# Optimization experiments

Measured on AMD Instinct MI355X. Metric: run time of the kernel, lower is better.

## Reference

```python
import jax, jax.numpy as jnp
import numpy as np

EPS = 1e-5
EMBED_DIM = 1024
CTX_DIM = 768
NUM_HEADS = 16
DH = EMBED_DIM // NUM_HEADS
# Faithful to torch source: embed_dim // num_heads ** 0.5 parses as embed_dim // (num_heads**0.5)
SCALE = EMBED_DIM // (NUM_HEADS ** 0.5)  # = 256.0


def ws_conv1x1(x, w, b, mask):
    # weight-standardized 1x1 conv1d: w [O, I, 1], x [B, I, T]
    w2 = w[..., 0]
    mu = jnp.mean(w2, axis=1, keepdims=True)
    var = jnp.var(w2, axis=1, keepdims=True)
    wn = (w2 - mu) * jax.lax.rsqrt(var + EPS)
    y = jnp.einsum('oi,bit->bot', wn, x) + b[None, :, None]
    if mask is not None:
        y = jnp.where(mask, y, 0.0)  # mask [B,1,T] bool
    return y


def layernorm(x, g, b):
    # normalize over last axis
    mu = jnp.mean(x, axis=-1, keepdims=True)
    var = jnp.var(x, axis=-1, keepdims=True)
    return (x - mu) * jax.lax.rsqrt(var + EPS) * g + b


def setup_inputs() -> dict:
    key = jax.random.key(0)
    ks = jax.random.split(key, 16)
    B, T, S = 4, 1024, 1024
    inp = {
        'x': jax.random.normal(ks[0], (B, EMBED_DIM, T), dtype=jnp.float32),
        'context': jax.random.normal(ks[1], (B, CTX_DIM, S), dtype=jnp.float32),
        'mask': jax.random.randint(ks[2], (B, 1, T), 0, 2).astype(bool),
        'mask_ctx': jax.random.randint(ks[3], (B, 1, S), 0, 2).astype(bool),
        'qw': jax.random.normal(ks[4], (EMBED_DIM, EMBED_DIM, 1), dtype=jnp.float32) * 0.02,
        'qb': jnp.zeros((EMBED_DIM,), jnp.float32),
        'kw': jax.random.normal(ks[5], (EMBED_DIM, CTX_DIM, 1), dtype=jnp.float32) * 0.02,
        'kb': jnp.zeros((EMBED_DIM,), jnp.float32),
        'vw': jax.random.normal(ks[6], (EMBED_DIM, CTX_DIM, 1), dtype=jnp.float32) * 0.02,
        'vb': jnp.zeros((EMBED_DIM,), jnp.float32),
        'ow': jax.random.normal(ks[7], (EMBED_DIM, EMBED_DIM, 1), dtype=jnp.float32) * 0.02,
        'ob': jnp.zeros((EMBED_DIM,), jnp.float32),
        'gq': jnp.ones((DH,), jnp.float32), 'bq': jnp.zeros((DH,), jnp.float32),
        'gk': jnp.ones((DH,), jnp.float32), 'bk': jnp.zeros((DH,), jnp.float32),
        'gv': jnp.ones((DH,), jnp.float32), 'bv': jnp.zeros((DH,), jnp.float32),
    }
    return inp


def reference(x, context, mask, mask_ctx, qw, qb, kw, kb, vw, vb, ow, ob, gq, bq, gk, bk, gv, bv):
    B, E, T = x.shape
    S = context.shape[-1]
    q = ws_conv1x1(x, qw, qb, mask)            # [B,E,T]
    k = ws_conv1x1(context, kw, kb, mask_ctx)  # [B,E,S]
    v = ws_conv1x1(context, vw, vb, mask_ctx)  # [B,E,S]
    # split heads -> [B,H,dh,L]
    q = q.reshape(B, NUM_HEADS, DH, T)
    k = k.reshape(B, NUM_HEADS, DH, S)
    v = v.reshape(B, NUM_HEADS, DH, S)
    # middle_norm: LayerNorm over dh (applied on transposed layout)
    q = jnp.swapaxes(layernorm(jnp.swapaxes(q, -1, -2), gq, bq), -1, -2)
    k = jnp.swapaxes(layernorm(jnp.swapaxes(k, -1, -2), gk, bk), -1, -2)
    v = jnp.swapaxes(layernorm(jnp.swapaxes(v, -1, -2), gv, bv), -1, -2)
    # scores: k^T @ q -> [B,H,S,T]
    scores = jnp.einsum('bhds,bhdt->bhst', k, q) / SCALE
    scores = jnp.where(mask[:, :, None, :], scores, -1e9)  # mask over query dim T
    scores = jax.nn.softmax(scores, axis=-1)               # softmax over T (as in source)
    scores = jnp.where(mask_ctx[:, :, :, None], scores, 0.0)
    out = jnp.einsum('bhds,bhst->bhdt', v, scores)          # v @ scores -> [B,H,dh,T]
    out = out.reshape(B, E, T)
    out = ws_conv1x1(out, ow, ob, mask) + x
    return out
```

## Files before the change

### kernel.cpp

```cpp
#include <hip/hip_runtime.h>

#define NB 4
#define TT 1024
#define SS 1024
#define EE 1024
#define CCH 768
#define NH 16
#define DHH 64
#define EPSF 1e-5f
#define QSCALE (1.4426950408889634f / 256.0f)

typedef unsigned short u16;
typedef __attribute__((ext_vector_type(8))) short short8;
typedef __attribute__((ext_vector_type(8))) unsigned short u16x8;
typedef __attribute__((ext_vector_type(4))) unsigned short u16x4;
typedef __attribute__((ext_vector_type(4))) float f32x4;

__device__ __forceinline__ u16 f2bu(float f) {
    union { float f; unsigned u; } x; x.f = f;
    unsigned r = x.u + 0x7fffu + ((x.u >> 16) & 1u);
    return (u16)(r >> 16);
}
__device__ __forceinline__ float bu2f(u16 u) {
    union { unsigned u; float f; } x; x.u = ((unsigned)u) << 16; return x.f;
}

#if __has_builtin(__builtin_amdgcn_exp2f)
#define EXP2(x) __builtin_amdgcn_exp2f(x)
#else
#define EXP2(x) exp2f(x)
#endif

#define MFMA16(a, b, c) __builtin_amdgcn_mfma_f32_16x16x32_bf16((a), (b), (c), 0, 0, 0)

__global__ __launch_bounds__(256) void ws_norm_scan(
    const float* __restrict__ qw, const float* __restrict__ kw,
    const float* __restrict__ vw, const float* __restrict__ ow,
    u16* __restrict__ wqn, u16* __restrict__ wkn,
    u16* __restrict__ wvn, u16* __restrict__ won,
    const int* __restrict__ mask, const int* __restrict__ mask_ctx,
    int* __restrict__ tIdx, int* __restrict__ sIdx,
    int* __restrict__ cntQ, int* __restrict__ cntK) {
    int tid = threadIdx.x;
    if (blockIdx.y == 4) {
        if (blockIdx.x >= 8) return;
        int which = blockIdx.x & 1, b = blockIdx.x >> 1;
        const int* m = (which ? mask_ctx : mask) + b * 1024;
        int* idx = (which ? sIdx : tIdx) + b * 1024;
        int* cnt = (which ? cntK : cntQ) + b;
        int base = tid * 4;
        int v[4]; int s = 0;
#pragma unroll
        for (int i = 0; i < 4; i++) { v[i] = m[base + i] ? 1 : 0; s += v[i]; }
        int lane = tid & 63, wid = tid >> 6;
        int inc = s;
#pragma unroll
        for (int off = 1; off < 64; off <<= 1) {
            int o = __shfl_up(inc, off);
            if (lane >= off) inc += o;
        }
        __shared__ int wtot[4];
        if (lane == 63) wtot[wid] = inc;
        __syncthreads();
        int woff = 0;
        for (int i = 0; i < wid; i++) woff += wtot[i];
        int p = woff + inc - s;
#pragma unroll
        for (int i = 0; i < 4; i++) {
            if (v[i]) idx[p] = base + i;
            p += v[i];
        }
        if (tid == 255) *cnt = p;
        return;
    }
    int mat = blockIdx.y;
    const float* w = mat == 0 ? qw : (mat == 1 ? kw : (mat == 2 ? vw : ow));
    u16* wn = mat == 0 ? wqn : (mat == 1 ? wkn : (mat == 2 ? wvn : won));
    int I = (mat == 1 || mat == 2) ? CCH : EE;
    int row = blockIdx.x;
    const float* wr = w + (size_t)row * I;
    float s = 0.f, s2 = 0.f;
    for (int i = tid; i < I; i += 256) { float v = wr[i]; s += v; s2 += v * v; }
#pragma unroll
    for (int off = 32; off > 0; off >>= 1) { s += __shfl_down(s, off); s2 += __shfl_down(s2, off); }
    __shared__ float sa[4], sb[4], smean, srstd;
    int wid = tid >> 6;
    if ((tid & 63) == 0) { sa[wid] = s; sb[wid] = s2; }
    __syncthreads();
    if (tid == 0) {
        float ts = sa[0] + sa[1] + sa[2] + sa[3];
        float ts2 = sb[0] + sb[1] + sb[2] + sb[3];
        float mean = ts / (float)I;
        float var = ts2 / (float)I - mean * mean;
        smean = mean; srstd = rsqrtf(var + EPSF);
    }
    __syncthreads();
    float mean = smean, r = srstd;
    u16* wo = wn + (size_t)row * I;
    for (int i = tid; i < I; i += 256) wo[i] = f2bu((wr[i] - mean) * r);
}

__global__ __launch_bounds__(256) void transpose2_compact(
    const float* __restrict__ x, const float* __restrict__ ctx,
    const int* __restrict__ mask, const int* __restrict__ mask_ctx,
    u16* __restrict__ xc, u16* __restrict__ cc) {
    __shared__ float tile[64][65];
    __shared__ int spos[64], smask[64], wtot[4];
    int yy = blockIdx.y;
    int mat = yy < 16 ? 0 : 1;
    int r0 = (mat == 0 ? yy : yy - 16) * 64;
    int R = mat == 0 ? EE : CCH;
    const float* in = mat == 0 ? x : ctx;
    const int* m = (mat == 0 ? mask : mask_ctx) + (size_t)blockIdx.z * 1024;
    u16* out = mat == 0 ? xc : cc;
    int c0 = blockIdx.x * 64, b = blockIdx.z;
    const float* ip = in + (size_t)b * R * 1024;
    u16* op = out + (size_t)b * R * 1024;
    int tid = threadIdx.x;
#pragma unroll
    for (int mm = 0; mm < 16; mm++) {
        int id = tid + 256 * mm; int r = id >> 6, c = id & 63;
        tile[r][c] = ip[(size_t)(r0 + r) * 1024 + c0 + c];
    }
    int base = tid * 4;
    int v[4]; int s = 0;
#pragma unroll
    for (int i = 0; i < 4; i++) { v[i] = m[base + i] ? 1 : 0; s += v[i]; }
    int lane = tid & 63, wid = tid >> 6;
    int inc = s;
#pragma unroll
    for (int off = 1; off < 64; off <<= 1) {
        int o = __shfl_up(inc, off);
        if (lane >= off) inc += o;
    }
    if (lane == 63) wtot[wid] = inc;
    __syncthreads();
    int woff = 0;
    for (int i = 0; i < wid; i++) woff += wtot[i];
    int p = woff + inc - s;
#pragma unroll
    for (int i = 0; i < 4; i++) {
        int g = base + i;
        if (g >= c0 && g < c0 + 64) { spos[g - c0] = p; smask[g - c0] = v[i]; }
        p += v[i];
    }
    __syncthreads();
#pragma unroll
    for (int mm = 0; mm < 16; mm++) {
        int id = tid + 256 * mm; int rr = id >> 6, cc2 = id & 63;
        if (smask[rr])
            op[(size_t)spos[rr] * R + r0 + cc2] = f2bu(tile[cc2][rr]);
    }
}

__device__ __forceinline__ void gemm_core(
    const u16* __restrict__ A, const u16* __restrict__ Bp, int I,
    int o0, int l0, u16 (*at)[72], u16 (*bt)[72], f32x4 (&acc)[4][2]) {
    int tid = threadIdx.x;
    int w = tid >> 6, lane = tid & 63, quad = lane >> 4, l16 = lane & 15;
    int wm = w & 1, wn = w >> 1;
    int rA = tid >> 3, cA = (tid & 7) * 8;
    u16x8 ra[2][4], rb[2][2];
#pragma unroll
    for (int p = 0; p < 2; p++) {
        int kb = p * 64;
#pragma unroll
        for (int m = 0; m < 4; m++)
            ra[p][m] = *(const u16x8*)&A[(size_t)(o0 + rA + 32 * m) * I + kb + cA];
#pragma unroll
        for (int m = 0; m < 2; m++)
            rb[p][m] = *(const u16x8*)&Bp[(size_t)(l0 + rA + 32 * m) * I + kb + cA];
    }
    for (int k0 = 0; k0 < I; k0 += 128) {
#pragma unroll
        for (int half = 0; half < 2; half++) {
            __syncthreads();
#pragma unroll
            for (int m = 0; m < 4; m++) *(u16x8*)&at[rA + 32 * m][cA] = ra[half][m];
#pragma unroll
            for (int m = 0; m < 2; m++) *(u16x8*)&bt[rA + 32 * m][cA] = rb[half][m];
            __syncthreads();
            int kpre = k0 + half * 64 + 128;
            if (kpre < I) {
#pragma unroll
                for (int m = 0; m < 4; m++)
                    ra[half][m] = *(const u16x8*)&A[(size_t)(o0 + rA + 32 * m) * I + kpre + cA];
#pragma unroll
                for (int m = 0; m < 2; m++)
                    rb[half][m] = *(const u16x8*)&Bp[(size_t)(l0 + rA + 32 * m) * I + kpre + cA];
            }
#pragma unroll
            for (int ks = 0; ks < 64; ks += 32) {
                short8 af[4], bf[2];
#pragma unroll
                for (int i = 0; i < 4; i++)
                    af[i] = *(const short8*)&at[wm * 64 + i * 16 + l16][ks + quad * 8];
#pragma unroll
                for (int j = 0; j < 2; j++)
                    bf[j] = *(const short8*)&bt[wn * 32 + j * 16 + l16][ks + quad * 8];
#pragma unroll
                for (int mt = 0; mt < 4; mt++)
#pragma unroll
                    for (int nt = 0; nt < 2; nt++)
                        acc[mt][nt] = MFMA16(af[mt], bf[nt], acc[mt][nt]);
            }
        }
    }
}

__global__ __launch_bounds__(256) void proj_qkv(
    const u16* __restrict__ wq, const u16* __restrict__ wk, const u16* __restrict__ wv,
    const u16* __restrict__ xc, const u16* __restrict__ cc,
    const float* __restrict__ qb, const float* __restrict__ kb, const float* __restrict__ vbi,
    const int* __restrict__ cntQ, const int* __restrict__ cntK,
    const float* __restrict__ gq, const float* __restrict__ bq,
    const float* __restrict__ gk, const float* __restrict__ bk,
    u16* __restrict__ qc, u16* __restrict__ kc, u16* __restrict__ yv) {
    int mat = blockIdx.y >> 3;
    int l0 = blockIdx.x * 64;
    int b = blockIdx.z;
    int limit = (mat == 0) ? cntQ[b] : cntK[b];
    if (l0 >= limit) return;
    __shared__ u16 at[128][72];
    __shared__ u16 bt[64][72];
    __shared__ float sg[64], sbe[64], sbias[128];
    int tid = threadIdx.x;
    int w = tid >> 6, lane = tid & 63, quad = lane >> 4, l16 = lane & 15;
    int wm = w & 1, wn = w >> 1;
    int o0 = (blockIdx.y & 7) * 128;
    const u16* A = mat == 0 ? wq : (mat == 1 ? wk : wv);
    const u16* BT = mat == 0 ? xc : cc;
    const float* bias = mat == 0 ? qb : (mat == 1 ? kb : vbi);
    int I = mat == 0 ? EE : CCH;
    if (mat < 2 && tid < 64) {
        sg[tid] = (mat == 0 ? gq : gk)[tid];
        sbe[tid] = (mat == 0 ? bq : bk)[tid];
    }
    if (tid < 128) sbias[tid] = bias[o0 + tid];

    f32x4 acc[4][2] = {};
    gemm_core(A, BT + (size_t)b * 1024 * I, I, o0, l0, at, bt, acc);

    if (mat < 2) {
        u16* outT = mat == 0 ? qc : kc;
        float scale = mat == 0 ? QSCALE : 1.0f;
        int h = (o0 >> 6) + wm;
        int bh = b * NH + h;
#pragma unroll
        for (int nt = 0; nt < 2; nt++) {
            int l = l0 + wn * 32 + nt * 16 + l16;
            float vbuf[16];
            float s = 0.f;
#pragma unroll
            for (int mt = 0; mt < 4; mt++)
#pragma unroll
                for (int reg = 0; reg < 4; reg++) {
                    float v = acc[mt][nt][reg] + sbias[wm * 64 + mt * 16 + quad * 4 + reg];
                    vbuf[mt * 4 + reg] = v; s += v;
                }
            s += __shfl_xor(s, 16); s += __shfl_xor(s, 32);
            float mean = s * (1.f / 64);
            float s2 = 0.f;
#pragma unroll
            for (int i = 0; i < 16; i++) { float dv = vbuf[i] - mean; s2 += dv * dv; }
            s2 += __shfl_xor(s2, 16); s2 += __shfl_xor(s2, 32);
            float r = rsqrtf(s2 * (1.f / 64) + EPSF);
            if (l < limit) {
                u16* op = outT + ((size_t)bh * 1024 + l) * 64;
#pragma unroll
                for (int mt = 0; mt < 4; mt++) {
                    u16x4 pk;
#pragma unroll
                    for (int reg = 0; reg < 4; reg++) {
                        int d = mt * 16 + quad * 4 + reg;
                        pk[reg] = f2bu(((vbuf[mt * 4 + reg] - mean) * r * sg[d] + sbe[d]) * scale);
                    }
                    *(u16x4*)&op[mt * 16 + quad * 4] = pk;
                }
            }
        }
    } else {
#pragma unroll
        for (int nt = 0; nt < 2; nt++) {
            int l = l0 + wn * 32 + nt * 16 + l16;
            if (l < limit) {
#pragma unroll
                for (int mt = 0; mt < 4; mt++)
#pragma unroll
                    for (int reg = 0; reg < 4; reg++) {
                        int o = o0 + wm * 64 + mt * 16 + quad * 4 + reg;
                        float v = acc[mt][nt][reg] + sbias[wm * 64 + mt * 16 + quad * 4 + reg];
                        yv[((size_t)b * EE + o) * 1024 + l] = f2bu(v);
                    }
            }
        }
    }
}

__global__ __launch_bounds__(256) void proj_o(
    const u16* __restrict__ won, const u16* __restrict__ aT,
    const float* __restrict__ obi, const int* __restrict__ mask,
    const float* __restrict__ x, float* __restrict__ out) {
    __shared__ u16 at[128][72];
    __shared__ u16 bt[64][72];
    __shared__ float sbias[128];
    int tid = threadIdx.x;
    int w = tid >> 6, lane = tid & 63, quad = lane >> 4, l16 = lane & 15;
    int wm = w & 1, wn = w >> 1;
    int o0 = blockIdx.y * 128, l0 = blockIdx.x * 64, b = blockIdx.z;
    if (tid < 128) sbias[tid] = obi[o0 + tid];
    f32x4 acc[4][2] = {};
    gemm_core(won, aT + (size_t)b * TT * EE, EE, o0, l0, at, bt, acc);
    const int* mrow = mask + (size_t)b * TT;
#pragma unroll
    for (int nt = 0; nt < 2; nt++) {
        int l = l0 + wn * 32 + nt * 16 + l16;
        int mval = mrow[l];
#pragma unroll
        for (int mt = 0; mt < 4; mt++)
#pragma unroll
            for (int reg = 0; reg < 4; reg++) {
                int o = o0 + wm * 64 + mt * 16 + quad * 4 + reg;
                float v = mval ? (acc[mt][nt][reg] + sbias[wm * 64 + mt * 16 + quad * 4 + reg]) : 0.f;
                size_t off = ((size_t)b * EE + o) * TT + l;
                out[off] = v + x[off];
            }
    }
}

__global__ __launch_bounds__(256) void attn_stats_mfma(
    const u16* __restrict__ qc, const u16* __restrict__ kc,
    const int* __restrict__ cntQ, const int* __restrict__ cntK,
    const float* __restrict__ gv, const float* __restrict__ bv,
    const u16* __restrict__ yv, u16* __restrict__ vc) {
    int s0 = blockIdx.x * 64, h = blockIdx.y, b = blockIdx.z;
    int Sc = cntK[b], Tc = cntQ[b];
    if (s0 >= Sc) return;
    __shared__ u16 kt[64][72];
    __shared__ u16 qt[64][72];
    __shared__ float lp[4][64];
    int tid = threadIdx.x;
    int w = tid >> 6, lane = tid & 63, quad = lane >> 4, l16 = lane & 15;
    int head = b * NH + h;
    const u16* kp = kc + (size_t)head * SS * DHH;
    const u16* qp = qc + (size_t)head * TT * DHH;
    int rA = tid >> 3, cA = (tid & 7) * 8;
#pragma unroll
    for (int m = 0; m < 2; m++)
        *(u16x8*)&kt[rA + 32 * m][cA] = *(const u16x8*)&kp[(size_t)(s0 + rA + 32 * m) * DHH + cA];
    u16x8 rq[2][2];
#pragma unroll
    for (int p = 0; p < 2; p++)
#pragma unroll
        for (int m = 0; m < 2; m++)
            rq[p][m] = *(const u16x8*)&qp[(size_t)(p * 64 + rA + 32 * m) * DHH + cA];
    float rl[4][4] = {};
    for (int t0 = 0; t0 < Tc; t0 += 128) {
#pragma unroll
        for (int half = 0; half < 2; half++) {
            int tb = t0 + half * 64;
            __syncthreads();
#pragma unroll
            for (int m = 0; m < 2; m++) *(u16x8*)&qt[rA + 32 * m][cA] = rq[half][m];
            __syncthreads();
            int tpre = tb + 128;
            if (tpre < TT) {
#pragma unroll
                for (int m = 0; m < 2; m++)
                    rq[half][m] = *(const u16x8*)&qp[(size_t)(tpre + rA + 32 * m) * DHH + cA];
            }
            int tcol = tb + w * 16 + l16;
            f32x4 acc[4] = {};
#pragma unroll
            for (int ks = 0; ks < 64; ks += 32) {
                short8 bf = *(const short8*)&qt[w * 16 + l16][ks + quad * 8];
#pragma unroll
                for (int mt = 0; mt < 4; mt++) {
                    short8 af = *(const short8*)&kt[mt * 16 + l16][ks + quad * 8];
                    acc[mt] = MFMA16(af, bf, acc[mt]);
                }
            }
            if (tcol < Tc) {
#pragma unroll
                for (int mt = 0; mt < 4; mt++)
#pragma unroll
                    for (int reg = 0; reg < 4; reg++)
                        rl[mt][reg] += EXP2(acc[mt][reg]);
            }
        }
    }
#pragma unroll
    for (int mt = 0; mt < 4; mt++) {
#pragma unroll
        for (int reg = 0; reg < 4; reg++) {
            float v = rl[mt][reg];
            v += __shfl_xor(v, 1); v += __shfl_xor(v, 2);
            v += __shfl_xor(v, 4); v += __shfl_xor(v, 8);
            if (l16 == 0) lp[w][mt * 16 + quad * 4 + reg] = v;
        }
    }
    __syncthreads();
    if (tid < 64 && s0 + tid < Sc) {
        int spos = s0 + tid;
        float lv = lp[0][tid] + lp[1][tid] + lp[2][tid] + lp[3][tid];
        float wsc = lv > 0.f ? (1.f / lv) : 0.f;
        const u16* vin = yv + ((size_t)b * EE + h * 64) * SS + spos;
        u16* vout = vc + ((size_t)b * EE + h * 64) * SS + spos;
        float sm = 0.f, s2 = 0.f;
        float vals[DHH];
#pragma unroll
        for (int d = 0; d < DHH; d++) {
            float v = bu2f(vin[(size_t)d * SS]);
            vals[d] = v; sm += v; s2 += v * v;
        }
        float mean = sm * (1.f / DHH);
        float var = s2 * (1.f / DHH) - mean * mean;
        float r = rsqrtf(var + EPSF);
#pragma unroll
        for (int d = 0; d < DHH; d++)
            vout[(size_t)d * SS] = f2bu(((vals[d] - mean) * r * gv[d] + bv[d]) * wsc);
    }
}

__global__ __launch_bounds__(256) void attn_pv_mfma(
    const u16* __restrict__ qc, const u16* __restrict__ kc, const u16* __restrict__ vc,
    const int* __restrict__ tIdx, const int* __restrict__ cntQ, const int* __restrict__ cntK,
    u16* __restrict__ aT) {
    int t0 = blockIdx.x * 64, h = blockIdx.y, b = blockIdx.z;
    int Tc = cntQ[b], Sc = cntK[b];
    if (t0 >= Tc) return;
    __shared__ u16 qt[64][72];
    __shared__ u16 kt[64][72];
    __shared__ u16 vt[64][72];
    __shared__ u16 pt[64][72];
    int tid = threadIdx.x;
    int w = tid >> 6, lane = tid & 63, quad = lane >> 4, l16 = lane & 15;
    int head = b * NH + h;
    const u16* qp = qc + (size_t)head * TT * DHH;
    const u16* kp = kc + (size_t)head * SS * DHH;
    const u16* vp = vc + ((size_t)head * DHH) * SS;
    int rA = tid >> 3, cA = (tid & 7) * 8;
#pragma unroll
    for (int m = 0; m < 2; m++)
        *(u16x8*)&qt[rA + 32 * m][cA] = *(const u16x8*)&qp[(size_t)(t0 + rA + 32 * m) * DHH + cA];
    u16x8 rk[2][2], rv[2][2];
#pragma unroll
    for (int p = 0; p < 2; p++)
#pragma unroll
        for (int m = 0; m < 2; m++) {
            rk[p][m] = *(const u16x8*)&kp[(size_t)(p * 64 + rA + 32 * m) * DHH + cA];
            rv[p][m] = *(const u16x8*)&vp[(size_t)(rA + 32 * m) * SS + p * 64 + cA];
        }
    int tl = w * 16 + l16;

    f32x4 oacc[4] = {};
    for (int s0 = 0; s0 < Sc; s0 += 128) {
#pragma unroll
        for (int half = 0; half < 2; half++) {
            int sb = s0 + half * 64;
            if (sb >= Sc) break;
            __syncthreads();
#pragma unroll
            for (int m = 0; m < 2; m++) {
                *(u16x8*)&kt[rA + 32 * m][cA] = rk[half][m];
                *(u16x8*)&vt[rA + 32 * m][cA] = rv[half][m];
            }
            __syncthreads();
            int spre = sb + 128;
            if (spre < SS) {
#pragma unroll
                for (int m = 0; m < 2; m++) {
                    rk[half][m] = *(const u16x8*)&kp[(size_t)(spre + rA + 32 * m) * DHH + cA];
                    rv[half][m] = *(const u16x8*)&vp[(size_t)(rA + 32 * m) * SS + spre + cA];
                }
            }
            f32x4 acc[4] = {};
#pragma unroll
            for (int ks = 0; ks < 64; ks += 32) {
                short8 bf = *(const short8*)&qt[tl][ks + quad * 8];
#pragma unroll
                for (int mt = 0; mt < 4; mt++) {
                    short8 af = *(const short8*)&kt[mt * 16 + l16][ks + quad * 8];
                    acc[mt] = MFMA16(af, bf, acc[mt]);
                }
            }
#pragma unroll
            for (int mt = 0; mt < 4; mt++) {
                u16x4 pk;
#pragma unroll
                for (int reg = 0; reg < 4; reg++) {
                    int sl = mt * 16 + quad * 4 + reg;
                    pk[reg] = (sb + sl < Sc) ? f2bu(EXP2(acc[mt][reg])) : (u16)0;
                }
                *(u16x4*)&pt[tl][mt * 16 + quad * 4] = pk;
            }
#pragma unroll
            for (int ks = 0; ks < 64; ks += 32) {
                short8 bf = *(const short8*)&pt[tl][ks + quad * 8];
#pragma unroll
                for (int mt = 0; mt < 4; mt++) {
                    short8 af = *(const short8*)&vt[mt * 16 + l16][ks + quad * 8];
                    oacc[mt] = MFMA16(af, bf, oacc[mt]);
                }
            }
        }
    }
    __syncthreads();
#pragma unroll
    for (int mt = 0; mt < 4; mt++) {
        u16x4 pk;
#pragma unroll
        for (int reg = 0; reg < 4; reg++) pk[reg] = f2bu(oacc[mt][reg]);
        *(u16x4*)&pt[tl][mt * 16 + quad * 4] = pk;
    }
    __syncthreads();
    const int* ti = tIdx + (size_t)b * 1024;
#pragma unroll
    for (int i = 0; i < 2; i++) {
        int id = tid * 2 + i;
        int r = id >> 3, c = (id & 7) * 8;
        if (t0 + r < Tc) {
            int treal = ti[t0 + r];
            *(u16x8*)&aT[((size_t)b * TT + treal) * EE + h * 64 + c] =
                *(const u16x8*)&pt[r][c];
        }
    }
}

extern "C" void kernel_launch(void* const* d_in, const int* in_sizes, int n_in,
                              void* d_out, int out_size, void* d_ws, size_t ws_size,
                              hipStream_t stream) {
    const float* x        = (const float*)d_in[0];
    const float* ctx      = (const float*)d_in[1];
    const int*   mask     = (const int*)d_in[2];
    const int*   mask_ctx = (const int*)d_in[3];
    const float* qw  = (const float*)d_in[4];
    const float* qbi = (const float*)d_in[5];
    const float* kw  = (const float*)d_in[6];
    const float* kbi = (const float*)d_in[7];
    const float* vw  = (const float*)d_in[8];
    const float* vbi = (const float*)d_in[9];
    const float* ow  = (const float*)d_in[10];
    const float* obi = (const float*)d_in[11];
    const float* gq = (const float*)d_in[12];
    const float* bq = (const float*)d_in[13];
    const float* gk = (const float*)d_in[14];
    const float* bk = (const float*)d_in[15];
    const float* gv = (const float*)d_in[16];
    const float* bv = (const float*)d_in[17];

    u16* p = (u16*)d_ws;
    u16* wqn = p; p += (size_t)EE * EE;
    u16* wkn = p; p += (size_t)EE * CCH;
    u16* wvn = p; p += (size_t)EE * CCH;
    u16* won = p; p += (size_t)EE * EE;
    u16* xc  = p; p += (size_t)NB * TT * EE;
    u16* cc  = p; p += (size_t)NB * SS * CCH;
    u16* yv  = p; p += (size_t)NB * EE * SS;
    u16* qc  = p; p += (size_t)NB * NH * TT * DHH;
    u16* kc  = p; p += (size_t)NB * NH * SS * DHH;
    u16* vc  = p; p += (size_t)NB * EE * SS;
    u16* aT  = p; p += (size_t)NB * TT * EE;
    int* tIdx = (int*)p;
    int* sIdx = tIdx + NB * 1024;
    int* cntQ = sIdx + NB * 1024;
    int* cntK = cntQ + NB;

    ws_norm_scan<<<dim3(1024, 5), 256, 0, stream>>>(
        qw, kw, vw, ow, wqn, wkn, wvn, won, mask, mask_ctx, tIdx, sIdx, cntQ, cntK);

    transpose2_compact<<<dim3(16, 28, NB), 256, 0, stream>>>(
        x, ctx, mask, mask_ctx, xc, cc);

    proj_qkv<<<dim3(16, 24, NB), 256, 0, stream>>>(
        wqn, wkn, wvn, xc, cc, qbi, kbi, vbi, cntQ, cntK,
        gq, bq, gk, bk, qc, kc, yv);

    attn_stats_mfma<<<dim3(16, NH, NB), 256, 0, stream>>>(
        qc, kc, cntQ, cntK, gv, bv, yv, vc);

    attn_pv_mfma<<<dim3(16, NH, NB), 256, 0, stream>>>(
        qc, kc, vc, tIdx, cntQ, cntK, aT);

    proj_o<<<dim3(16, 8, NB), 256, 0, stream>>>(won, aT, obi, mask, x, (float*)d_out);
}
```

Measured before the change: 232.7 us.

## Fuse prep kernels, compact output projection over valid queries, prefill masked outputs

Merges weight standardization, mask scan and transpose/compaction into a single prep launch that also writes the residual x into masked output positions. The output projection now runs on compacted attention rows and skips tiles beyond the valid query count, scattering results to real time positions via the index table. It uses a smaller 64x64 GEMM tile with more blocks. proj_qkv grid axes are swapped for a different block ordering. The scattered output writes are less coalesced, and the prep kernel branches heavily across block types.

```diff
diff --git a/kernel.cpp b/kernel.cpp
--- a/kernel.cpp
+++ b/kernel.cpp
@@ -33,18 +33,56 @@
 
 #define MFMA16(a, b, c) __builtin_amdgcn_mfma_f32_16x16x32_bf16((a), (b), (c), 0, 0, 0)
 
-__global__ __launch_bounds__(256) void ws_norm_scan(
+#define PREP_WS_END   4096
+#define PREP_SCAN_END (PREP_WS_END + 8)
+#define PREP_TR_END   (PREP_SCAN_END + 1792)
+#define PREP_FILL_END (PREP_TR_END + 4096)
+
+__global__ __launch_bounds__(256) void prep(
     const float* __restrict__ qw, const float* __restrict__ kw,
     const float* __restrict__ vw, const float* __restrict__ ow,
     u16* __restrict__ wqn, u16* __restrict__ wkn,
     u16* __restrict__ wvn, u16* __restrict__ won,
+    const float* __restrict__ x, const float* __restrict__ ctx,
     const int* __restrict__ mask, const int* __restrict__ mask_ctx,
+    u16* __restrict__ xc, u16* __restrict__ cc,
     int* __restrict__ tIdx, int* __restrict__ sIdx,
-    int* __restrict__ cntQ, int* __restrict__ cntK) {
-    int tid = threadIdx.x;
-    if (blockIdx.y == 4) {
-        if (blockIdx.x >= 8) return;
-        int which = blockIdx.x & 1, b = blockIdx.x >> 1;
+    int* __restrict__ cntQ, int* __restrict__ cntK,
+    float* __restrict__ outF) {
+    __shared__ float tile[64][65];
+    __shared__ int spos[64], smask[64], wtoti[4];
+    __shared__ float sa[4], sb2[4], smean, srstd;
+    int bid = blockIdx.x, tid = threadIdx.x;
+
+    if (bid < PREP_WS_END) {
+        int mat = bid >> 10, row = bid & 1023;
+        const float* w = mat == 0 ? qw : (mat == 1 ? kw : (mat == 2 ? vw : ow));
+        u16* wn = mat == 0 ? wqn : (mat == 1 ? wkn : (mat == 2 ? wvn : won));
+        int I = (mat == 1 || mat == 2) ? CCH : EE;
+        const float* wr = w + (size_t)row * I;
+        float s = 0.f, s2 = 0.f;
+        for (int i = tid; i < I; i += 256) { float v = wr[i]; s += v; s2 += v * v; }
+#pragma unroll
+        for (int off = 32; off > 0; off >>= 1) { s += __shfl_down(s, off); s2 += __shfl_down(s2, off); }
+        int wid = tid >> 6;
+        if ((tid & 63) == 0) { sa[wid] = s; sb2[wid] = s2; }
+        __syncthreads();
+        if (tid == 0) {
+            float ts = sa[0] + sa[1] + sa[2] + sa[3];
+            float ts2 = sb2[0] + sb2[1] + sb2[2] + sb2[3];
+            float mean = ts / (float)I;
+            float var = ts2 / (float)I - mean * mean;
+            smean = mean; srstd = rsqrtf(var + EPSF);
+        }
+        __syncthreads();
+        float mean = smean, r = srstd;
+        u16* wo = wn + (size_t)row * I;
+        for (int i = tid; i < I; i += 256) wo[i] = f2bu((wr[i] - mean) * r);
+        return;
+    }
+    if (bid < PREP_SCAN_END) {
+        int t = bid - PREP_WS_END;
+        int which = t & 1, b = t >> 1;
         const int* m = (which ? mask_ctx : mask) + b * 1024;
         int* idx = (which ? sIdx : tIdx) + b * 1024;
         int* cnt = (which ? cntK : cntQ) + b;
@@ -59,11 +97,10 @@
             int o = __shfl_up(inc, off);
             if (lane >= off) inc += o;
         }
-        __shared__ int wtot[4];
-        if (lane == 63) wtot[wid] = inc;
+        if (lane == 63) wtoti[wid] = inc;
         __syncthreads();
         int woff = 0;
-        for (int i = 0; i < wid; i++) woff += wtot[i];
+        for (int i = 0; i < wid; i++) woff += wtoti[i];
         int p = woff + inc - s;
 #pragma unroll
         for (int i = 0; i < 4; i++) {
@@ -73,83 +110,68 @@
         if (tid == 255) *cnt = p;
         return;
     }
-    int mat = blockIdx.y;
-    const float* w = mat == 0 ? qw : (mat == 1 ? kw : (mat == 2 ? vw : ow));
-    u16* wn = mat == 0 ? wqn : (mat == 1 ? wkn : (mat == 2 ? wvn : won));
-    int I = (mat == 1 || mat == 2) ? CCH : EE;
-    int row = blockIdx.x;
-    const float* wr = w + (size_t)row * I;
-    float s = 0.f, s2 = 0.f;
-    for (int i = tid; i < I; i += 256) { float v = wr[i]; s += v; s2 += v * v; }
-#pragma unroll
-    for (int off = 32; off > 0; off >>= 1) { s += __shfl_down(s, off); s2 += __shfl_down(s2, off); }
-    __shared__ float sa[4], sb[4], smean, srstd;
-    int wid = tid >> 6;
-    if ((tid & 63) == 0) { sa[wid] = s; sb[wid] = s2; }
-    __syncthreads();
-    if (tid == 0) {
-        float ts = sa[0] + sa[1] + sa[2] + sa[3];
-        float ts2 = sb[0] + sb[1] + sb[2] + sb[3];
-        float mean = ts / (float)I;
-        float var = ts2 / (float)I - mean * mean;
-        smean = mean; srstd = rsqrtf(var + EPSF);
-    }
-    __syncthreads();
-    float mean = smean, r = srstd;
-    u16* wo = wn + (size_t)row * I;
-    for (int i = tid; i < I; i += 256) wo[i] = f2bu((wr[i] - mean) * r);
-}
-
-__global__ __launch_bounds__(256) void transpose2_compact(
-    const float* __restrict__ x, const float* __restrict__ ctx,
-    const int* __restrict__ mask, const int* __restrict__ mask_ctx,
-    u16* __restrict__ xc, u16* __restrict__ cc) {
-    __shared__ float tile[64][65];
-    __shared__ int spos[64], smask[64], wtot[4];
-    int yy = blockIdx.y;
-    int mat = yy < 16 ? 0 : 1;
-    int r0 = (mat == 0 ? yy : yy - 16) * 64;
-    int R = mat == 0 ? EE : CCH;
-    const float* in = mat == 0 ? x : ctx;
-    const int* m = (mat == 0 ? mask : mask_ctx) + (size_t)blockIdx.z * 1024;
-    u16* out = mat == 0 ? xc : cc;
-    int c0 = blockIdx.x * 64, b = blockIdx.z;
-    const float* ip = in + (size_t)b * R * 1024;
-    u16* op = out + (size_t)b * R * 1024;
-    int tid = threadIdx.x;
-#pragma unroll
-    for (int mm = 0; mm < 16; mm++) {
-        int id = tid + 256 * mm; int r = id >> 6, c = id & 63;
-        tile[r][c] = ip[(size_t)(r0 + r) * 1024 + c0 + c];
-    }
-    int base = tid * 4;
-    int v[4]; int s = 0;
-#pragma unroll
-    for (int i = 0; i < 4; i++) { v[i] = m[base + i] ? 1 : 0; s += v[i]; }
-    int lane = tid & 63, wid = tid >> 6;
-    int inc = s;
-#pragma unroll
-    for (int off = 1; off < 64; off <<= 1) {
-        int o = __shfl_up(inc, off);
-        if (lane >= off) inc += o;
-    }
-    if (lane == 63) wtot[wid] = inc;
-    __syncthreads();
-    int woff = 0;
-    for (int i = 0; i < wid; i++) woff += wtot[i];
-    int p = woff + inc - s;
-#pragma unroll
-    for (int i = 0; i < 4; i++) {
-        int g = base + i;
-        if (g >= c0 && g < c0 + 64) { spos[g - c0] = p; smask[g - c0] = v[i]; }
-        p += v[i];
-    }
-    __syncthreads();
-#pragma unroll
-    for (int mm = 0; mm < 16; mm++) {
-        int id = tid + 256 * mm; int rr = id >> 6, cc2 = id & 63;
-        if (smask[rr])
-            op[(size_t)spos[rr] * R + r0 + cc2] = f2bu(tile[cc2][rr]);
+    if (bid < PREP_TR_END) {
+        int t = bid - PREP_SCAN_END;
+        int xb = t & 15; int rem = t >> 4;
+        int yy = rem % 28, b = rem / 28;
+        int mat = yy < 16 ? 0 : 1;
+        int r0 = (mat == 0 ? yy : yy - 16) * 64;
+        int R = mat == 0 ? EE : CCH;
+        const float* in = mat == 0 ? x : ctx;
+        const int* m = (mat == 0 ? mask : mask_ctx) + (size_t)b * 1024;
+        u16* out = mat == 0 ? xc : cc;
+        int c0 = xb * 64;
+        const float* ip = in + (size_t)b * R * 1024;
+        u16* op = out + (size_t)b * R * 1024;
+#pragma unroll
+        for (int mm = 0; mm < 16; mm++) {
+            int id = tid + 256 * mm; int r = id >> 6, c = id & 63;
+            tile[r][c] = ip[(size_t)(r0 + r) * 1024 + c0 + c];
+        }
+        int base = tid * 4;
+        int v[4]; int s = 0;
+#pragma unroll
+        for (int i = 0; i < 4; i++) { v[i] = m[base + i] ? 1 : 0; s += v[i]; }
+        int lane = tid & 63, wid = tid >> 6;
+        int inc = s;
+#pragma unroll
+        for (int off = 1; off < 64; off <<= 1) {
+            int o = __shfl_up(inc, off);
+            if (lane >= off) inc += o;
+        }
+        if (lane == 63) wtoti[wid] = inc;
+        __syncthreads();
+        int woff = 0;
+        for (int i = 0; i < wid; i++) woff += wtoti[i];
+        int p = woff + inc - s;
+#pragma unroll
+        for (int i = 0; i < 4; i++) {
+            int g = base + i;
+            if (g >= c0 && g < c0 + 64) { spos[g - c0] = p; smask[g - c0] = v[i]; }
+            p += v[i];
+        }
+        __syncthreads();
+#pragma unroll
+        for (int mm = 0; mm < 16; mm++) {
+            int id = tid + 256 * mm; int rr = id >> 6, cc2 = id & 63;
+            if (smask[rr])
+                op[(size_t)spos[rr] * R + r0 + cc2] = f2bu(tile[cc2][rr]);
+        }
+        return;
+    }
+    {
+        int f = bid - PREP_TR_END;
+        int b = f >> 10, o = f & 1023;
+        const float* xr = x + ((size_t)b * EE + o) * TT;
+        float* orow = outF + ((size_t)b * EE + o) * TT;
+        const int* mrow = mask + (size_t)b * TT;
+        int4 mv = ((const int4*)mrow)[tid];
+        float4 xv = ((const float4*)xr)[tid];
+        int t4 = tid * 4;
+        if (!mv.x) orow[t4 + 0] = xv.x;
+        if (!mv.y) orow[t4 + 1] = xv.y;
+        if (!mv.z) orow[t4 + 2] = xv.z;
+        if (!mv.w) orow[t4 + 3] = xv.w;
     }
 }
 
@@ -208,6 +230,53 @@
     }
 }
 
+__device__ __forceinline__ void gemm_core64(
+    const u16* __restrict__ A, const u16* __restrict__ Bp, int I,
+    int o0, int l0, u16 (*at)[72], u16 (*bt)[72], f32x4 (&acc)[4]) {
+    int tid = threadIdx.x;
+    int w = tid >> 6, lane = tid & 63, quad = lane >> 4, l16 = lane & 15;
+    int rA = tid >> 3, cA = (tid & 7) * 8;
+    u16x8 ra[2][2], rb[2][2];
+#pragma unroll
+    for (int p = 0; p < 2; p++) {
+        int kb = p * 64;
+#pragma unroll
+        for (int m = 0; m < 2; m++) {
+            ra[p][m] = *(const u16x8*)&A[(size_t)(o0 + rA + 32 * m) * I + kb + cA];
+            rb[p][m] = *(const u16x8*)&Bp[(size_t)(l0 + rA + 32 * m) * I + kb + cA];
+        }
+    }
+    for (int k0 = 0; k0 < I; k0 += 128) {
+#pragma unroll
+        for (int half = 0; half < 2; half++) {
+            __syncthreads();
+#pragma unroll
+            for (int m = 0; m < 2; m++) {
+                *(u16x8*)&at[rA + 32 * m][cA] = ra[half][m];
+                *(u16x8*)&bt[rA + 32 * m][cA] = rb[half][m];
+            }
+            __syncthreads();
+            int kpre = k0 + half * 64 + 128;
+            if (kpre < I) {
+#pragma unroll
+                for (int m = 0; m < 2; m++) {
+                    ra[half][m] = *(const u16x8*)&A[(size_t)(o0 + rA + 32 * m) * I + kpre + cA];
+                    rb[half][m] = *(const u16x8*)&Bp[(size_t)(l0 + rA + 32 * m) * I + kpre + cA];
+                }
+            }
+#pragma unroll
+            for (int ks = 0; ks < 64; ks += 32) {
+                short8 bf = *(const short8*)&bt[w * 16 + l16][ks + quad * 8];
+#pragma unroll
+                for (int mt = 0; mt < 4; mt++) {
+                    short8 af = *(const short8*)&at[mt * 16 + l16][ks + quad * 8];
+                    acc[mt] = MFMA16(af, bf, acc[mt]);
+                }
+            }
+        }
+    }
+}
+
 __global__ __launch_bounds__(256) void proj_qkv(
     const u16* __restrict__ wq, const u16* __restrict__ wk, const u16* __restrict__ wv,
     const u16* __restrict__ xc, const u16* __restrict__ cc,
@@ -216,8 +285,9 @@
     const float* __restrict__ gq, const float* __restrict__ bq,
     const float* __restrict__ gk, const float* __restrict__ bk,
     u16* __restrict__ qc, u16* __restrict__ kc, u16* __restrict__ yv) {
-    int mat = blockIdx.y >> 3;
-    int l0 = blockIdx.x * 64;
+    int mat = blockIdx.x >> 3;
+    int o0 = (blockIdx.x & 7) * 128;
+    int l0 = blockIdx.y * 64;
     int b = blockIdx.z;
     int limit = (mat == 0) ? cntQ[b] : cntK[b];
     if (l0 >= limit) return;
@@ -227,7 +297,6 @@
     int tid = threadIdx.x;
     int w = tid >> 6, lane = tid & 63, quad = lane >> 4, l16 = lane & 15;
     int wm = w & 1, wn = w >> 1;
-    int o0 = (blockIdx.y & 7) * 128;
     const u16* A = mat == 0 ? wq : (mat == 1 ? wk : wv);
     const u16* BT = mat == 0 ? xc : cc;
     const float* bias = mat == 0 ? qb : (mat == 1 ? kb : vbi);
@@ -294,37 +363,6 @@
                     }
             }
         }
-    }
-}
-
-__global__ __launch_bounds__(256) void proj_o(
-    const u16* __restrict__ won, const u16* __restrict__ aT,
-    const float* __restrict__ obi, const int* __restrict__ mask,
-    const float* __restrict__ x, float* __restrict__ out) {
-    __shared__ u16 at[128][72];
-    __shared__ u16 bt[64][72];
-    __shared__ float sbias[128];
-    int tid = threadIdx.x;
-    int w = tid >> 6, lane = tid & 63, quad = lane >> 4, l16 = lane & 15;
-    int wm = w & 1, wn = w >> 1;
-    int o0 = blockIdx.y * 128, l0 = blockIdx.x * 64, b = blockIdx.z;
-    if (tid < 128) sbias[tid] = obi[o0 + tid];
-    f32x4 acc[4][2] = {};
-    gemm_core(won, aT + (size_t)b * TT * EE, EE, o0, l0, at, bt, acc);
-    const int* mrow = mask + (size_t)b * TT;
-#pragma unroll
-    for (int nt = 0; nt < 2; nt++) {
-        int l = l0 + wn * 32 + nt * 16 + l16;
-        int mval = mrow[l];
-#pragma unroll
-        for (int mt = 0; mt < 4; mt++)
-#pragma unroll
-            for (int reg = 0; reg < 4; reg++) {
-                int o = o0 + wm * 64 + mt * 16 + quad * 4 + reg;
-                float v = mval ? (acc[mt][nt][reg] + sbias[wm * 64 + mt * 16 + quad * 4 + reg]) : 0.f;
-                size_t off = ((size_t)b * EE + o) * TT + l;
-                out[off] = v + x[off];
-            }
     }
 }
 
@@ -424,8 +462,8 @@
 
 __global__ __launch_bounds__(256) void attn_pv_mfma(
     const u16* __restrict__ qc, const u16* __restrict__ kc, const u16* __restrict__ vc,
-    const int* __restrict__ tIdx, const int* __restrict__ cntQ, const int* __restrict__ cntK,
-    u16* __restrict__ aT) {
+    const int* __restrict__ cntQ, const int* __restrict__ cntK,
+    u16* __restrict__ ac) {
     int t0 = blockIdx.x * 64, h = blockIdx.y, b = blockIdx.z;
     int Tc = cntQ[b], Sc = cntK[b];
     if (t0 >= Tc) return;
@@ -514,16 +552,47 @@
         *(u16x4*)&pt[tl][mt * 16 + quad * 4] = pk;
     }
     __syncthreads();
-    const int* ti = tIdx + (size_t)b * 1024;
 #pragma unroll
     for (int i = 0; i < 2; i++) {
         int id = tid * 2 + i;
         int r = id >> 3, c = (id & 7) * 8;
-        if (t0 + r < Tc) {
-            int treal = ti[t0 + r];
-            *(u16x8*)&aT[((size_t)b * TT + treal) * EE + h * 64 + c] =
+        if (t0 + r < Tc)
+            *(u16x8*)&ac[((size_t)b * TT + t0 + r) * EE + h * 64 + c] =
                 *(const u16x8*)&pt[r][c];
-        }
+    }
+}
+
+__global__ __launch_bounds__(256) void proj_o(
+    const u16* __restrict__ won, const u16* __restrict__ ac,
+    const float* __restrict__ obi, const int* __restrict__ tIdx,
+    const int* __restrict__ cntQ, const float* __restrict__ x,
+    float* __restrict__ out) {
+    int o0 = blockIdx.x * 64, l0 = blockIdx.y * 64, b = blockIdx.z;
+    int Tc = cntQ[b];
+    if (l0 >= Tc) return;
+    __shared__ u16 at[64][72];
+    __shared__ u16 bt[64][72];
+    __shared__ float sbias[64];
+    __shared__ int stre[64];
+    int tid = threadIdx.x;
+    int w = tid >> 6, lane = tid & 63, quad = lane >> 4, l16 = lane & 15;
+    if (tid < 64) {
+        sbias[tid] = obi[o0 + tid];
+        stre[tid] = tIdx[(size_t)b * 1024 + l0 + tid];
+    }
+    f32x4 acc[4] = {};
+    gemm_core64(won, ac + (size_t)b * TT * EE, EE, o0, l0, at, bt, acc);
+    int l = l0 + w * 16 + l16;
+    if (l < Tc) {
+        int treal = stre[w * 16 + l16];
+#pragma unroll
+        for (int mt = 0; mt < 4; mt++)
+#pragma unroll
+            for (int reg = 0; reg < 4; reg++) {
+                int o = o0 + mt * 16 + quad * 4 + reg;
+                size_t off = ((size_t)b * EE + o) * TT + treal;
+                out[off] = acc[mt][reg] + sbias[mt * 16 + quad * 4 + reg] + x[off];
+            }
     }
 }
 
@@ -560,19 +629,17 @@
     u16* qc  = p; p += (size_t)NB * NH * TT * DHH;
     u16* kc  = p; p += (size_t)NB * NH * SS * DHH;
     u16* vc  = p; p += (size_t)NB * EE * SS;
-    u16* aT  = p; p += (size_t)NB * TT * EE;
+    u16* ac  = p; p += (size_t)NB * TT * EE;
     int* tIdx = (int*)p;
     int* sIdx = tIdx + NB * 1024;
     int* cntQ = sIdx + NB * 1024;
     int* cntK = cntQ + NB;
 
-    ws_norm_scan<<<dim3(1024, 5), 256, 0, stream>>>(
-        qw, kw, vw, ow, wqn, wkn, wvn, won, mask, mask_ctx, tIdx, sIdx, cntQ, cntK);
-
-    transpose2_compact<<<dim3(16, 28, NB), 256, 0, stream>>>(
-        x, ctx, mask, mask_ctx, xc, cc);
-
-    proj_qkv<<<dim3(16, 24, NB), 256, 0, stream>>>(
+    prep<<<PREP_FILL_END, 256, 0, stream>>>(
+        qw, kw, vw, ow, wqn, wkn, wvn, won, x, ctx, mask, mask_ctx,
+        xc, cc, tIdx, sIdx, cntQ, cntK, (float*)d_out);
+
+    proj_qkv<<<dim3(24, 16, NB), 256, 0, stream>>>(
         wqn, wkn, wvn, xc, cc, qbi, kbi, vbi, cntQ, cntK,
         gq, bq, gk, bk, qc, kc, yv);
 
@@ -580,7 +647,8 @@
         qc, kc, cntQ, cntK, gv, bv, yv, vc);
 
     attn_pv_mfma<<<dim3(16, NH, NB), 256, 0, stream>>>(
-        qc, kc, vc, tIdx, cntQ, cntK, aT);
-
-    proj_o<<<dim3(16, 8, NB), 256, 0, stream>>>(won, aT, obi, mask, x, (float*)d_out);
-}
+        qc, kc, vc, cntQ, cntK, ac);
+
+    proj_o<<<dim3(16, 16, NB), 256, 0, stream>>>(
+        won, ac, obi, tIdx, cntQ, x, (float*)d_out);
+}
```

Result: faster. 223.7 us (-3.9%).
